# Kernel optimization log

Hardware: AMD Instinct MI355X
Metric: run time of the kernel (lower is better)

The kernel has to match this reference:

```python
import jax, jax.numpy as jnp
import numpy as np

B, N, K = 4, 65536, 16
HIDDEN = 64


def setup_inputs() -> dict:
    key = jax.random.key(0)
    k1, k2, k3, k4 = jax.random.split(key, 4)
    pos = jax.random.normal(k1, (B, 3, N), dtype=jnp.float32)
    idx = jax.random.randint(k2, (B, N, K), 0, N, dtype=jnp.int64)
    dist = jax.random.uniform(k3, (B, N, K), dtype=jnp.float32)
    W = jax.random.normal(k4, (10, HIDDEN), dtype=jnp.float32) * (1.0 / np.sqrt(10.0))
    b = jnp.zeros((HIDDEN,), dtype=jnp.float32)
    return {"pos": pos, "idx": idx, "dist": dist, "W": W, "b": b}


def reference(pos, idx, dist, W, b):
    xyz = pos[:, :3, :]                                  # [B, 3, N]
    # gather neighbor coords: neighbors[b, c, n, k] = xyz[b, c, idx[b, n, k]]
    neighbors = jax.vmap(lambda x, i: x[:, i])(xyz, idx)  # [B, 3, N, K]
    ext_xyz = jnp.broadcast_to(xyz[:, :, :, None], neighbors.shape)
    concat = jnp.concatenate(
        [ext_xyz, neighbors, ext_xyz - neighbors, dist[:, None, :, :]], axis=1
    )                                                    # [B, 10, N, K]
    feat = jnp.max(concat, axis=-1)                      # [B, 10, N]
    feat = jnp.transpose(feat, (0, 2, 1))                # [B, N, 10]
    return jax.nn.relu(feat @ W + b)                     # [B, N, HIDDEN]
```

## Files before the change

### kernel.cpp

```cpp
#include <hip/hip_runtime.h>

#define NPTS 65536
#define NB_SHIFT 16
#define KNBR 16
#define HID 64

typedef int   i32x4 __attribute__((ext_vector_type(4)));
typedef float f32x4 __attribute__((ext_vector_type(4)));

__global__ __launch_bounds__(256) void xyzt_kernel(const float* __restrict__ pos,
                                                   float4* __restrict__ xyzt) {
    const int tid = threadIdx.x;
    const int blk = ((int)blockIdx.x & 7) * 128 + ((int)blockIdx.x >> 3);
    const int g = blk * 256 + tid;
    const int b = g >> NB_SHIFT;
    const int n = g & (NPTS - 1);
    const float* p = pos + (size_t)b * 3 * NPTS;
    float4 v;
    v.x = __builtin_nontemporal_load(p + n);
    v.y = __builtin_nontemporal_load(p + n + NPTS);
    v.z = __builtin_nontemporal_load(p + n + 2 * NPTS);
    v.w = 0.f;
    xyzt[((size_t)b << NB_SHIFT) + n] = v;
}

template <int USE_T>
__global__ __launch_bounds__(256) void point_embed_kernel(
    const float*  __restrict__ pos,
    const float4* __restrict__ xyzt,
    const int*    __restrict__ idx,
    const float*  __restrict__ dist,
    const float*  __restrict__ W,
    const float*  __restrict__ bias,
    float*        __restrict__ out) {
    __shared__ float feat[10][257];
    const int tid = threadIdx.x;

    const int blk = ((int)blockIdx.x & 7) * 128 + ((int)blockIdx.x >> 3);
    const int g = blk * 256 + tid;
    const int b = g >> NB_SHIFT;
    const int n = g & (NPTS - 1);

    const int hq = tid & 15;
    float4 Wv[10];
#pragma unroll
    for (int c = 0; c < 10; ++c)
        Wv[c] = ((const float4*)(W + c * HID))[hq];
    const float4 bv = ((const float4*)bias)[hq];

    const i32x4* iv = (const i32x4*)idx + (size_t)g * 4;
    i32x4 i0 = __builtin_nontemporal_load(iv + 0);
    i32x4 i1 = __builtin_nontemporal_load(iv + 1);
    i32x4 i2 = __builtin_nontemporal_load(iv + 2);
    i32x4 i3 = __builtin_nontemporal_load(iv + 3);
    const f32x4* dv = (const f32x4*)dist + (size_t)g * 4;
    f32x4 d0 = __builtin_nontemporal_load(dv + 0);
    f32x4 d1 = __builtin_nontemporal_load(dv + 1);
    f32x4 d2 = __builtin_nontemporal_load(dv + 2);
    f32x4 d3 = __builtin_nontemporal_load(dv + 3);
    float maxd = fmaxf(
        fmaxf(fmaxf(fmaxf(d0.x, d0.y), fmaxf(d0.z, d0.w)),
              fmaxf(fmaxf(d1.x, d1.y), fmaxf(d1.z, d1.w))),
        fmaxf(fmaxf(fmaxf(d2.x, d2.y), fmaxf(d2.z, d2.w)),
              fmaxf(fmaxf(d3.x, d3.y), fmaxf(d3.z, d3.w))));

    float cx, cy, cz;
    float mxx = -INFINITY, mxy = -INFINITY, mxz = -INFINITY;
    float mnx = INFINITY, mny = INFINITY, mnz = INFINITY;

    if (USE_T) {
        const float4* xb = xyzt + ((size_t)b << NB_SHIFT);
        float4 c = xb[n];
        cx = c.x; cy = c.y; cz = c.z;
#define GATH(J)                                   \
    {                                             \
        float4 q = xb[(J)];                       \
        mxx = fmaxf(mxx, q.x);                    \
        mxy = fmaxf(mxy, q.y);                    \
        mxz = fmaxf(mxz, q.z);                    \
        mnx = fminf(mnx, q.x);                    \
        mny = fminf(mny, q.y);                    \
        mnz = fminf(mnz, q.z);                    \
    }
        GATH(i0.x) GATH(i0.y) GATH(i0.z) GATH(i0.w)
        GATH(i1.x) GATH(i1.y) GATH(i1.z) GATH(i1.w)
        GATH(i2.x) GATH(i2.y) GATH(i2.z) GATH(i2.w)
        GATH(i3.x) GATH(i3.y) GATH(i3.z) GATH(i3.w)
#undef GATH
    } else {
        const float* px = pos + (size_t)b * 3 * NPTS;
        cx = px[n]; cy = px[n + NPTS]; cz = px[n + 2 * NPTS];
#define GATH(J)                                   \
    {                                             \
        float qx = px[(J)];                       \
        float qy = px[(J) + NPTS];                \
        float qz = px[(J) + 2 * NPTS];            \
        mxx = fmaxf(mxx, qx);                     \
        mxy = fmaxf(mxy, qy);                     \
        mxz = fmaxf(mxz, qz);                     \
        mnx = fminf(mnx, qx);                     \
        mny = fminf(mny, qy);                     \
        mnz = fminf(mnz, qz);                     \
    }
        GATH(i0.x) GATH(i0.y) GATH(i0.z) GATH(i0.w)
        GATH(i1.x) GATH(i1.y) GATH(i1.z) GATH(i1.w)
        GATH(i2.x) GATH(i2.y) GATH(i2.z) GATH(i2.w)
        GATH(i3.x) GATH(i3.y) GATH(i3.z) GATH(i3.w)
#undef GATH
    }

    feat[0][tid] = cx;
    feat[1][tid] = cy;
    feat[2][tid] = cz;
    feat[3][tid] = mxx;
    feat[4][tid] = mxy;
    feat[5][tid] = mxz;
    feat[6][tid] = cx - mnx;
    feat[7][tid] = cy - mny;
    feat[8][tid] = cz - mnz;
    feat[9][tid] = maxd;
    __syncthreads();

    const int prow = tid >> 4;
    const size_t outbase = (size_t)blk * 256 * HID;
#pragma unroll
    for (int i = 0; i < 16; ++i) {
        const int p = i * 16 + prow;
        float4 acc = bv;
#pragma unroll
        for (int c = 0; c < 10; ++c) {
            const float fv = feat[c][p];
            acc.x += fv * Wv[c].x;
            acc.y += fv * Wv[c].y;
            acc.z += fv * Wv[c].z;
            acc.w += fv * Wv[c].w;
        }
        f32x4 av;
        av.x = fmaxf(acc.x, 0.f);
        av.y = fmaxf(acc.y, 0.f);
        av.z = fmaxf(acc.z, 0.f);
        av.w = fmaxf(acc.w, 0.f);
        __builtin_nontemporal_store(av,
            (f32x4*)(out + outbase + (size_t)p * HID) + hq);
    }
}

extern "C" void kernel_launch(void* const* d_in, const int* in_sizes, int n_in,
                              void* d_out, int out_size, void* d_ws, size_t ws_size,
                              hipStream_t stream) {
    const float* pos  = (const float*)d_in[0];
    const int*   idx  = (const int*)d_in[1];
    const float* dist = (const float*)d_in[2];
    const float* W    = (const float*)d_in[3];
    const float* bias = (const float*)d_in[4];
    float* out = (float*)d_out;

    const int total   = in_sizes[0] / 3;
    const int nblocks = total / 256;
    const size_t need = (size_t)total * sizeof(float4);

    if (ws_size >= need) {
        xyzt_kernel<<<nblocks, 256, 0, stream>>>(pos, (float4*)d_ws);
        point_embed_kernel<1><<<nblocks, 256, 0, stream>>>(
            pos, (const float4*)d_ws, idx, dist, W, bias, out);
    } else {
        point_embed_kernel<0><<<nblocks, 256, 0, stream>>>(
            pos, nullptr, idx, dist, W, bias, out);
    }
}
```

Baseline: 128.8 us.

## Split each point's neighbor gather across two threads with shuffle reduction

Assigns two threads per point, each loading half of the indices and distances and gathering eight neighbours, then combines the partial max/min via lane xor shuffles. Blocks now cover 128 points, with twice as many blocks launched. This aims to raise memory-level parallelism for the random gathers. In exchange, the centre-point load is duplicated and there is extra shuffle work.

```diff
diff --git a/kernel.cpp b/kernel.cpp
--- a/kernel.cpp
+++ b/kernel.cpp
@@ -4,6 +4,7 @@
 #define NB_SHIFT 16
 #define KNBR 16
 #define HID 64
+#define PPB 128
 
 typedef int   i32x4 __attribute__((ext_vector_type(4)));
 typedef float f32x4 __attribute__((ext_vector_type(4)));
@@ -33,11 +34,13 @@
     const float*  __restrict__ W,
     const float*  __restrict__ bias,
     float*        __restrict__ out) {
-    __shared__ float feat[10][257];
+    __shared__ float feat[10][PPB];
     const int tid = threadIdx.x;
 
-    const int blk = ((int)blockIdx.x & 7) * 128 + ((int)blockIdx.x >> 3);
-    const int g = blk * 256 + tid;
+    const int blk = ((int)blockIdx.x & 7) * 256 + ((int)blockIdx.x >> 3);
+    const int p = tid >> 1;
+    const int h = tid & 1;
+    const int g = blk * PPB + p;
     const int b = g >> NB_SHIFT;
     const int n = g & (NPTS - 1);
 
@@ -48,21 +51,14 @@
         Wv[c] = ((const float4*)(W + c * HID))[hq];
     const float4 bv = ((const float4*)bias)[hq];
 
-    const i32x4* iv = (const i32x4*)idx + (size_t)g * 4;
+    const i32x4* iv = (const i32x4*)idx + (size_t)g * 4 + h * 2;
     i32x4 i0 = __builtin_nontemporal_load(iv + 0);
     i32x4 i1 = __builtin_nontemporal_load(iv + 1);
-    i32x4 i2 = __builtin_nontemporal_load(iv + 2);
-    i32x4 i3 = __builtin_nontemporal_load(iv + 3);
-    const f32x4* dv = (const f32x4*)dist + (size_t)g * 4;
+    const f32x4* dv = (const f32x4*)dist + (size_t)g * 4 + h * 2;
     f32x4 d0 = __builtin_nontemporal_load(dv + 0);
     f32x4 d1 = __builtin_nontemporal_load(dv + 1);
-    f32x4 d2 = __builtin_nontemporal_load(dv + 2);
-    f32x4 d3 = __builtin_nontemporal_load(dv + 3);
-    float maxd = fmaxf(
-        fmaxf(fmaxf(fmaxf(d0.x, d0.y), fmaxf(d0.z, d0.w)),
-              fmaxf(fmaxf(d1.x, d1.y), fmaxf(d1.z, d1.w))),
-        fmaxf(fmaxf(fmaxf(d2.x, d2.y), fmaxf(d2.z, d2.w)),
-              fmaxf(fmaxf(d3.x, d3.y), fmaxf(d3.z, d3.w))));
+    float maxd = fmaxf(fmaxf(fmaxf(d0.x, d0.y), fmaxf(d0.z, d0.w)),
+                       fmaxf(fmaxf(d1.x, d1.y), fmaxf(d1.z, d1.w)));
 
     float cx, cy, cz;
     float mxx = -INFINITY, mxy = -INFINITY, mxz = -INFINITY;
@@ -84,8 +80,6 @@
     }
         GATH(i0.x) GATH(i0.y) GATH(i0.z) GATH(i0.w)
         GATH(i1.x) GATH(i1.y) GATH(i1.z) GATH(i1.w)
-        GATH(i2.x) GATH(i2.y) GATH(i2.z) GATH(i2.w)
-        GATH(i3.x) GATH(i3.y) GATH(i3.z) GATH(i3.w)
 #undef GATH
     } else {
         const float* px = pos + (size_t)b * 3 * NPTS;
@@ -104,32 +98,40 @@
     }
         GATH(i0.x) GATH(i0.y) GATH(i0.z) GATH(i0.w)
         GATH(i1.x) GATH(i1.y) GATH(i1.z) GATH(i1.w)
-        GATH(i2.x) GATH(i2.y) GATH(i2.z) GATH(i2.w)
-        GATH(i3.x) GATH(i3.y) GATH(i3.z) GATH(i3.w)
 #undef GATH
     }
 
-    feat[0][tid] = cx;
-    feat[1][tid] = cy;
-    feat[2][tid] = cz;
-    feat[3][tid] = mxx;
-    feat[4][tid] = mxy;
-    feat[5][tid] = mxz;
-    feat[6][tid] = cx - mnx;
-    feat[7][tid] = cy - mny;
-    feat[8][tid] = cz - mnz;
-    feat[9][tid] = maxd;
+    mxx = fmaxf(mxx, __shfl_xor(mxx, 1));
+    mxy = fmaxf(mxy, __shfl_xor(mxy, 1));
+    mxz = fmaxf(mxz, __shfl_xor(mxz, 1));
+    mnx = fminf(mnx, __shfl_xor(mnx, 1));
+    mny = fminf(mny, __shfl_xor(mny, 1));
+    mnz = fminf(mnz, __shfl_xor(mnz, 1));
+    maxd = fmaxf(maxd, __shfl_xor(maxd, 1));
+
+    if (h == 0) {
+        feat[0][p] = cx;
+        feat[1][p] = cy;
+        feat[2][p] = cz;
+        feat[3][p] = mxx;
+        feat[4][p] = mxy;
+        feat[5][p] = mxz;
+        feat[6][p] = cx - mnx;
+        feat[7][p] = cy - mny;
+        feat[8][p] = cz - mnz;
+        feat[9][p] = maxd;
+    }
     __syncthreads();
 
     const int prow = tid >> 4;
-    const size_t outbase = (size_t)blk * 256 * HID;
+    const size_t outbase = (size_t)blk * PPB * HID;
 #pragma unroll
-    for (int i = 0; i < 16; ++i) {
-        const int p = i * 16 + prow;
+    for (int i = 0; i < 8; ++i) {
+        const int pp = i * 16 + prow;
         float4 acc = bv;
 #pragma unroll
         for (int c = 0; c < 10; ++c) {
-            const float fv = feat[c][p];
+            const float fv = feat[c][pp];
             acc.x += fv * Wv[c].x;
             acc.y += fv * Wv[c].y;
             acc.z += fv * Wv[c].z;
@@ -141,7 +143,7 @@
         av.z = fmaxf(acc.z, 0.f);
         av.w = fmaxf(acc.w, 0.f);
         __builtin_nontemporal_store(av,
-            (f32x4*)(out + outbase + (size_t)p * HID) + hq);
+            (f32x4*)(out + outbase + (size_t)pp * HID) + hq);
     }
 }
 
@@ -155,16 +157,15 @@
     const float* bias = (const float*)d_in[4];
     float* out = (float*)d_out;
 
-    const int total   = in_sizes[0] / 3;
-    const int nblocks = total / 256;
+    const int total = in_sizes[0] / 3;
     const size_t need = (size_t)total * sizeof(float4);
 
     if (ws_size >= need) {
-        xyzt_kernel<<<nblocks, 256, 0, stream>>>(pos, (float4*)d_ws);
-        point_embed_kernel<1><<<nblocks, 256, 0, stream>>>(
+        xyzt_kernel<<<total / 256, 256, 0, stream>>>(pos, (float4*)d_ws);
+        point_embed_kernel<1><<<total / PPB, 256, 0, stream>>>(
             pos, (const float4*)d_ws, idx, dist, W, bias, out);
     } else {
-        point_embed_kernel<0><<<nblocks, 256, 0, stream>>>(
+        point_embed_kernel<0><<<total / PPB, 256, 0, stream>>>(
             pos, nullptr, idx, dist, W, bias, out);
     }
 }
```

New measurement: 126.5 us. About the same (-1.8%).
